# Kernel optimization log

Hardware: AMD Instinct MI355X
Metric: run time of the kernel (lower is better)

The kernel has to match this reference:

```python
import jax, jax.numpy as jnp
import numpy as np

HEADS, OUT_C = 8, 16
NEG_SLOPE = 0.2  # PyG GATConv default negative_slope


def setup_inputs() -> dict:
    key = jax.random.key(0)
    ks = jax.random.split(key, 6)
    N, E, IN = 100000, 1600000, 128
    x = jax.random.normal(ks[0], (N, IN), jnp.float32)
    edge_index = jax.random.randint(ks[1], (2, E), 0, N, dtype=jnp.int32)
    W = jax.random.normal(ks[2], (IN, HEADS * OUT_C), jnp.float32) / np.float32(np.sqrt(IN))
    att_src = jax.random.normal(ks[3], (HEADS, OUT_C), jnp.float32) * 0.1
    att_dst = jax.random.normal(ks[4], (HEADS, OUT_C), jnp.float32) * 0.1
    bias = jax.random.normal(ks[5], (HEADS * OUT_C,), jnp.float32) * 0.01
    return {"x": x, "edge_index": edge_index, "W": W,
            "att_src": att_src, "att_dst": att_dst, "bias": bias}


def reference(x, edge_index, W, att_src, att_dst, bias):
    N = x.shape[0]
    # Linear projection, split into heads: [N, H, C]
    xw = (x @ W).reshape(N, HEADS, OUT_C)
    # Add self-loops (PyG default add_self_loops=True)
    loops = jnp.arange(N, dtype=edge_index.dtype)
    src = jnp.concatenate([edge_index[0], loops])
    dst = jnp.concatenate([edge_index[1], loops])
    # Per-node attention terms [N, H], then per-edge logits
    a_s = jnp.einsum('nhc,hc->nh', xw, att_src)
    a_d = jnp.einsum('nhc,hc->nh', xw, att_dst)
    e = a_s[src] + a_d[dst]                       # [Etot, H]
    e = jnp.where(e > 0, e, NEG_SLOPE * e)        # LeakyReLU
    # Segment softmax over edges grouped by destination node
    emax = jax.ops.segment_max(e, dst, num_segments=N)
    p = jnp.exp(e - emax[dst])
    denom = jax.ops.segment_sum(p, dst, num_segments=N)
    alpha = p / (denom[dst] + 1e-16)              # [Etot, H]
    # Weighted scatter-aggregate of source messages
    out = jax.ops.segment_sum(xw[src] * alpha[:, :, None], dst, num_segments=N)
    out = out.reshape(N, HEADS * OUT_C) + bias    # concat heads + bias
    return jax.nn.relu(out)                       # act='relu', norm=None
```

## Files before the change

kernel.cpp:

```cpp
#include <hip/hip_runtime.h>
#include <math.h>

#define HEADS 8
#define OUTC 16
#define HC 128
#define NEG_SLOPE 0.2f

#define BM 128
#define BK 32
#define XPAD 132
#define CAP 64

typedef unsigned int uint;
typedef unsigned short ushort;

__device__ __forceinline__ ushort f2bf(float f) {
    uint u = __float_as_uint(f);
    u += 0x7FFFu + ((u >> 16) & 1u);
    return (ushort)(u >> 16);
}

__global__ __launch_bounds__(256, 4) void k_fused(
    const float* __restrict__ x, const float* __restrict__ W,
    const float* __restrict__ att_src, const float* __restrict__ att_dst,
    const int* __restrict__ ei,
    ushort* __restrict__ xwh, float* __restrict__ a_s, float* __restrict__ a_d,
    int* __restrict__ deg, int* __restrict__ csr,
    int N, int E, int GB) {
    __shared__ float xs[BK][XPAD];
    __shared__ float Ws[BK][XPAD];

    if (blockIdx.x >= GB) {
        int e = (blockIdx.x - GB) * 256 + threadIdx.x;
        if (e < E) {
            int src = ei[e];
            int dst = ei[E + e];
            int slot = atomicAdd(&deg[dst], 1);
            if (slot < CAP) csr[(size_t)dst * CAP + slot] = src;
        }
        return;
    }

    int t = threadIdx.x;
    int nb0 = blockIdx.x * BM;
    int tc = t & 15;
    int tr = t >> 4;

    float acc[8][8];
#pragma unroll
    for (int i = 0; i < 8; ++i)
#pragma unroll
        for (int j = 0; j < 8; ++j) acc[i][j] = 0.0f;

    for (int k0 = 0; k0 < HC; k0 += BK) {
        int kk4 = (t & 7) * 4;
#pragma unroll
        for (int p = 0; p < 4; ++p) {
            int nr = (t >> 3) + p * 32;
            int node = nb0 + nr;
            float4 v = make_float4(0.f, 0.f, 0.f, 0.f);
            if (node < N) v = *(const float4*)&x[(size_t)node * HC + k0 + kk4];
            xs[kk4 + 0][nr] = v.x;
            xs[kk4 + 1][nr] = v.y;
            xs[kk4 + 2][nr] = v.z;
            xs[kk4 + 3][nr] = v.w;
        }
        int kk = t >> 3;
        int c4 = (t & 7) * 4;
#pragma unroll
        for (int j = 0; j < 4; ++j) {
            *(float4*)&Ws[kk][c4 + j * 32] =
                *(const float4*)&W[(size_t)(k0 + kk) * HC + c4 + j * 32];
        }
        __syncthreads();

#pragma unroll 4
        for (int k = 0; k < BK; ++k) {
            float xa[8], wa[8];
            *(float4*)&xa[0] = *(const float4*)&xs[k][tr * 8];
            *(float4*)&xa[4] = *(const float4*)&xs[k][tr * 8 + 4];
            *(float4*)&wa[0] = *(const float4*)&Ws[k][tc * 8];
            *(float4*)&wa[4] = *(const float4*)&Ws[k][tc * 8 + 4];
#pragma unroll
            for (int i = 0; i < 8; ++i)
#pragma unroll
                for (int j = 0; j < 8; ++j)
                    acc[i][j] = fmaf(xa[i], wa[j], acc[i][j]);
        }
        __syncthreads();
    }

    float as8[8], ad8[8];
#pragma unroll
    for (int j = 0; j < 8; ++j) {
        as8[j] = att_src[tc * 8 + j];
        ad8[j] = att_dst[tc * 8 + j];
    }
    int h = tc >> 1;
#pragma unroll
    for (int i = 0; i < 8; ++i) {
        int node = nb0 + tr * 8 + i;
        float vs = 0.f, vd = 0.f;
        ushort h8[8];
#pragma unroll
        for (int j = 0; j < 8; ++j) {
            vs = fmaf(acc[i][j], as8[j], vs);
            vd = fmaf(acc[i][j], ad8[j], vd);
            h8[j] = f2bf(acc[i][j]);
        }
        vs += __shfl_xor(vs, 1);
        vd += __shfl_xor(vd, 1);
        if (node < N) {
            *(uint4*)&xwh[(size_t)node * HC + tc * 8] = *(uint4*)&h8[0];
            if ((tc & 1) == 0) {
                a_s[node * HEADS + h] = vs;
                a_d[node * HEADS + h] = vd;
            }
        }
    }
}

__global__ __launch_bounds__(256) void k_node(
    const int* __restrict__ deg, const int* __restrict__ csr,
    const float* __restrict__ a_s, const float* __restrict__ a_d,
    const uint* __restrict__ xwh, const float* __restrict__ bias,
    float* __restrict__ out, int N) {
    int n = blockIdx.x * 4 + (threadIdx.x >> 6);
    if (n >= N) return;
    int l = threadIdx.x & 63;
    int hB = l >> 3;

    float asn = a_s[n * HEADS + hB];
    float adn = a_d[n * HEADS + hB];

    float v = asn + adn;
    v = v > 0.0f ? v : NEG_SLOPE * v;
    float p = __expf(v);
    float den = p;
    uint w = xwh[n * 64 + l];
    float acc0 = p * __uint_as_float(w << 16);
    float acc1 = p * __uint_as_float(w & 0xFFFF0000u);

    int cnt = deg[n];
    if (cnt > CAP) cnt = CAP;
    const int* row = csr + (size_t)n * CAP;
#pragma unroll 4
    for (int i = 0; i < cnt; ++i) {
        int s = row[i];
        float vv = a_s[s * HEADS + hB] + adn;
        vv = vv > 0.0f ? vv : NEG_SLOPE * vv;
        float pp = __expf(vv);
        den += pp;
        uint ww = xwh[s * 64 + l];
        acc0 = fmaf(pp, __uint_as_float(ww << 16), acc0);
        acc1 = fmaf(pp, __uint_as_float(ww & 0xFFFF0000u), acc1);
    }

    float inv = 1.0f / (den + 1e-16f);
    float2 b = *(const float2*)&bias[2 * l];
    float r0 = acc0 * inv + b.x;
    float r1 = acc1 * inv + b.y;
    float2 o;
    o.x = r0 > 0.0f ? r0 : 0.0f;
    o.y = r1 > 0.0f ? r1 : 0.0f;
    *(float2*)&out[(size_t)n * HC + 2 * l] = o;
}

extern "C" void kernel_launch(void* const* d_in, const int* in_sizes, int n_in,
                              void* d_out, int out_size, void* d_ws, size_t ws_size,
                              hipStream_t stream) {
    const float* x       = (const float*)d_in[0];
    const int*   ei      = (const int*)d_in[1];
    const float* W       = (const float*)d_in[2];
    const float* att_src = (const float*)d_in[3];
    const float* att_dst = (const float*)d_in[4];
    const float* bias    = (const float*)d_in[5];
    float* out = (float*)d_out;

    int N = in_sizes[0] / HC;
    int E = in_sizes[1] / 2;

    ushort* xwh = (ushort*)d_ws;
    float* a_s  = (float*)(xwh + (size_t)N * HC);
    float* a_d  = a_s + (size_t)N * HEADS;
    int* deg    = (int*)(a_d + (size_t)N * HEADS);
    int* csr    = deg + N;

    hipMemsetAsync(deg, 0, (size_t)N * sizeof(int), stream);

    int GB = (N + BM - 1) / BM;
    int SB = (E + 255) / 256;
    k_fused<<<GB + SB, 256, 0, stream>>>(x, W, att_src, att_dst, ei,
                                         xwh, a_s, a_d, deg, csr, N, E, GB);

    k_node<<<(N + 3) / 4, 256, 0, stream>>>(deg, csr, a_s, a_d,
                                            (const uint*)xwh, bias, out, N);
}
```

Baseline: 278.0 us.

## Use bf16 MFMA for projection with attention vectors folded into weights

Replaces the fp32 FMA tiled GEMM with bf16 MFMA 16x16x32 instructions. A new prep kernel converts W to bf16 in MFMA fragment order and appends a ninth column tile holding W·att_src and W·att_dst, so the per-node attention logits come out of the same matrix multiply. x is converted to bf16 in shared memory, and the k_node unroll is raised to 8. This adds an extra small launch and lowers the precision of x, W and the attention logits to bf16, which could shift the softmax weights.

```diff
diff --git a/kernel.cpp b/kernel.cpp
--- a/kernel.cpp
+++ b/kernel.cpp
@@ -2,17 +2,18 @@
 #include <math.h>
 
 #define HEADS 8
-#define OUTC 16
 #define HC 128
 #define NEG_SLOPE 0.2f
 
-#define BM 128
-#define BK 32
-#define XPAD 132
+#define BM 64
+#define NT 9
+#define XS_STRIDE 136
 #define CAP 64
 
 typedef unsigned int uint;
 typedef unsigned short ushort;
+typedef __attribute__((ext_vector_type(8))) short bf16x8;
+typedef __attribute__((ext_vector_type(4))) float f32x4;
 
 __device__ __forceinline__ ushort f2bf(float f) {
     uint u = __float_as_uint(f);
@@ -20,18 +21,49 @@
     return (ushort)(u >> 16);
 }
 
-__global__ __launch_bounds__(256, 4) void k_fused(
-    const float* __restrict__ x, const float* __restrict__ W,
-    const float* __restrict__ att_src, const float* __restrict__ att_dst,
+__global__ void k_prep(const float* __restrict__ W, const float* __restrict__ att_src,
+                       const float* __restrict__ att_dst, ushort* __restrict__ Wb) {
+    int idx = blockIdx.x * 256 + threadIdx.x;
+    if (idx >= NT * 4 * 64) return;
+    int l = idx & 63;
+    int js = idx >> 6;
+    int s = js & 3;
+    int j = js >> 2;
+    int k0 = s * 32 + (l >> 4) * 8;
+    int c = l & 15;
+    ushort v[8];
+#pragma unroll
+    for (int jj = 0; jj < 8; ++jj) {
+        int k = k0 + jj;
+        float val;
+        if (j < 8) {
+            val = W[(size_t)k * HC + j * 16 + c];
+        } else {
+            int h = c & 7;
+            const float* att = (c < 8) ? att_src : att_dst;
+            float acc = 0.0f;
+#pragma unroll
+            for (int cc = 0; cc < 16; ++cc)
+                acc = fmaf(W[(size_t)k * HC + h * 16 + cc], att[h * 16 + cc], acc);
+            val = acc;
+        }
+        v[jj] = f2bf(val);
+    }
+    *(uint4*)&Wb[(size_t)idx * 8] = *(uint4*)&v[0];
+}
+
+__global__ __launch_bounds__(256) void k_fused(
+    const float* __restrict__ x, const ushort* __restrict__ Wb,
     const int* __restrict__ ei,
     ushort* __restrict__ xwh, float* __restrict__ a_s, float* __restrict__ a_d,
     int* __restrict__ deg, int* __restrict__ csr,
     int N, int E, int GB) {
-    __shared__ float xs[BK][XPAD];
-    __shared__ float Ws[BK][XPAD];
+    __shared__ __align__(16) ushort xs[BM * XS_STRIDE];
+
+    int t = threadIdx.x;
 
     if (blockIdx.x >= GB) {
-        int e = (blockIdx.x - GB) * 256 + threadIdx.x;
+        int e = (blockIdx.x - GB) * 256 + t;
         if (e < E) {
             int src = ei[e];
             int dst = ei[E + e];
@@ -41,81 +73,52 @@
         return;
     }
 
-    int t = threadIdx.x;
     int nb0 = blockIdx.x * BM;
-    int tc = t & 15;
-    int tr = t >> 4;
-
-    float acc[8][8];
-#pragma unroll
-    for (int i = 0; i < 8; ++i)
-#pragma unroll
-        for (int j = 0; j < 8; ++j) acc[i][j] = 0.0f;
-
-    for (int k0 = 0; k0 < HC; k0 += BK) {
-        int kk4 = (t & 7) * 4;
-#pragma unroll
-        for (int p = 0; p < 4; ++p) {
-            int nr = (t >> 3) + p * 32;
-            int node = nb0 + nr;
+
+    {
+        int r = t >> 2;
+        int node = nb0 + r;
+        int cb = (t & 3) * 4;
+#pragma unroll
+        for (int q = 0; q < 8; ++q) {
+            int col = cb + 16 * q;
             float4 v = make_float4(0.f, 0.f, 0.f, 0.f);
-            if (node < N) v = *(const float4*)&x[(size_t)node * HC + k0 + kk4];
-            xs[kk4 + 0][nr] = v.x;
-            xs[kk4 + 1][nr] = v.y;
-            xs[kk4 + 2][nr] = v.z;
-            xs[kk4 + 3][nr] = v.w;
-        }
-        int kk = t >> 3;
-        int c4 = (t & 7) * 4;
-#pragma unroll
-        for (int j = 0; j < 4; ++j) {
-            *(float4*)&Ws[kk][c4 + j * 32] =
-                *(const float4*)&W[(size_t)(k0 + kk) * HC + c4 + j * 32];
-        }
-        __syncthreads();
-
-#pragma unroll 4
-        for (int k = 0; k < BK; ++k) {
-            float xa[8], wa[8];
-            *(float4*)&xa[0] = *(const float4*)&xs[k][tr * 8];
-            *(float4*)&xa[4] = *(const float4*)&xs[k][tr * 8 + 4];
-            *(float4*)&wa[0] = *(const float4*)&Ws[k][tc * 8];
-            *(float4*)&wa[4] = *(const float4*)&Ws[k][tc * 8 + 4];
-#pragma unroll
-            for (int i = 0; i < 8; ++i)
-#pragma unroll
-                for (int j = 0; j < 8; ++j)
-                    acc[i][j] = fmaf(xa[i], wa[j], acc[i][j]);
-        }
-        __syncthreads();
-    }
-
-    float as8[8], ad8[8];
-#pragma unroll
-    for (int j = 0; j < 8; ++j) {
-        as8[j] = att_src[tc * 8 + j];
-        ad8[j] = att_dst[tc * 8 + j];
-    }
-    int h = tc >> 1;
-#pragma unroll
-    for (int i = 0; i < 8; ++i) {
-        int node = nb0 + tr * 8 + i;
-        float vs = 0.f, vd = 0.f;
-        ushort h8[8];
-#pragma unroll
-        for (int j = 0; j < 8; ++j) {
-            vs = fmaf(acc[i][j], as8[j], vs);
-            vd = fmaf(acc[i][j], ad8[j], vd);
-            h8[j] = f2bf(acc[i][j]);
-        }
-        vs += __shfl_xor(vs, 1);
-        vd += __shfl_xor(vd, 1);
+            if (node < N) v = *(const float4*)&x[(size_t)node * HC + col];
+            ushort h4[4] = {f2bf(v.x), f2bf(v.y), f2bf(v.z), f2bf(v.w)};
+            *(uint2*)&xs[r * XS_STRIDE + col] = *(uint2*)&h4[0];
+        }
+    }
+    __syncthreads();
+
+    int w = t >> 6;
+    int l = t & 63;
+    int m = l & 15;
+    int kq = l >> 4;
+
+    f32x4 acc[NT];
+#pragma unroll
+    for (int j = 0; j < NT; ++j) acc[j] = (f32x4){0.f, 0.f, 0.f, 0.f};
+
+#pragma unroll
+    for (int s = 0; s < 4; ++s) {
+        bf16x8 af = *(const bf16x8*)&xs[(w * 16 + m) * XS_STRIDE + s * 32 + kq * 8];
+#pragma unroll
+        for (int j = 0; j < NT; ++j) {
+            bf16x8 bf = *(const bf16x8*)&Wb[(size_t)((j * 4 + s) * 64 + l) * 8];
+            acc[j] = __builtin_amdgcn_mfma_f32_16x16x32_bf16(af, bf, acc[j], 0, 0, 0);
+        }
+    }
+
+#pragma unroll
+    for (int r = 0; r < 4; ++r) {
+        int node = nb0 + w * 16 + kq * 4 + r;
         if (node < N) {
-            *(uint4*)&xwh[(size_t)node * HC + tc * 8] = *(uint4*)&h8[0];
-            if ((tc & 1) == 0) {
-                a_s[node * HEADS + h] = vs;
-                a_d[node * HEADS + h] = vd;
-            }
+#pragma unroll
+            for (int j = 0; j < 8; ++j)
+                xwh[(size_t)node * HC + j * 16 + m] = f2bf(acc[j][r]);
+            float av = acc[8][r];
+            if (m < 8) a_s[node * HEADS + m] = av;
+            else       a_d[node * HEADS + (m - 8)] = av;
         }
     }
 }
@@ -144,7 +147,7 @@
     int cnt = deg[n];
     if (cnt > CAP) cnt = CAP;
     const int* row = csr + (size_t)n * CAP;
-#pragma unroll 4
+#pragma unroll 8
     for (int i = 0; i < cnt; ++i) {
         int s = row[i];
         float vv = a_s[s * HEADS + hB] + adn;
@@ -185,13 +188,16 @@
     float* a_d  = a_s + (size_t)N * HEADS;
     int* deg    = (int*)(a_d + (size_t)N * HEADS);
     int* csr    = deg + N;
+    ushort* Wb  = (ushort*)(csr + (size_t)N * CAP);
 
     hipMemsetAsync(deg, 0, (size_t)N * sizeof(int), stream);
+
+    k_prep<<<(NT * 4 * 64 + 255) / 256, 256, 0, stream>>>(W, att_src, att_dst, Wb);
 
     int GB = (N + BM - 1) / BM;
     int SB = (E + 255) / 256;
-    k_fused<<<GB + SB, 256, 0, stream>>>(x, W, att_src, att_dst, ei,
-                                         xwh, a_s, a_d, deg, csr, N, E, GB);
+    k_fused<<<GB + SB, 256, 0, stream>>>(x, Wb, ei, xwh, a_s, a_d,
+                                         deg, csr, N, E, GB);
 
     k_node<<<(N + 3) / 4, 256, 0, stream>>>(deg, csr, a_s, a_d,
                                             (const uint*)xwh, bias, out, N);
```

Result: slower. 288.7 us (+3.9%).
